# Kernel tuning notes

Hardware: AMD Instinct MI355X
Metric: run time of the kernel (lower is better)

The kernel has to match this reference:

```python
import jax, jax.numpy as jnp
import numpy as np

N_NODES = 50000
N_EDGES = 500000
D_FEAT = 128


def setup_inputs() -> dict:
    key = jax.random.key(0)
    k1, k2 = jax.random.split(key)
    x = jax.random.normal(k1, (N_NODES, D_FEAT), dtype=jnp.float32)
    edge_index = jax.random.randint(k2, (2, N_EDGES), 0, N_NODES, dtype=jnp.int64)
    return {"x": x, "edge_index": edge_index}


def reference(x, edge_index):
    # flow='source_to_target': row = edge_index[0] (source j), col = edge_index[1] (target i)
    row, col = edge_index[0], edge_index[1]
    # message(x_j) = x_j ; aggregate = scatter-add at target indices ; update = identity
    messages = jnp.take(x, row, axis=0)            # [E, D] gather
    out = jax.ops.segment_sum(messages, col, num_segments=x.shape[0])  # [N, D]
    return out
```

## Files before the change

### kernel.cpp

```cpp
#include <hip/hip_runtime.h>
#include <hip/hip_bf16.h>


#define D_FEAT 128
#define MAXDEG 32

typedef unsigned short u16;
typedef unsigned int u32;

__device__ __forceinline__ u16 f2bf(float f) {
    union { __hip_bfloat16 h; u16 u; } c;
    c.h = __float2bfloat16(f);
    return c.u;
}
__device__ __forceinline__ float bflo(u32 u) { return __uint_as_float(u << 16); }
__device__ __forceinline__ float bfhi(u32 u) { return __uint_as_float(u & 0xffff0000u); }

__global__ __launch_bounds__(256) void fused_kernel(const float* __restrict__ x,
                                                    u16* __restrict__ xb, int nf4,
                                                    const int* __restrict__ row,
                                                    const int* __restrict__ col,
                                                    int* __restrict__ cnt,
                                                    u16* __restrict__ srclist,
                                                    int* __restrict__ ovf,
                                                    int* __restrict__ ovfcnt,
                                                    int E, int ovfcap,
                                                    int fill_blocks, int aligned) {
    if ((int)blockIdx.x < fill_blocks) {
        const int t = blockIdx.x * 256 + threadIdx.x;
        const int e0 = t * 4;
        if (e0 >= E) return;
        int d[4], s[4], p[4], ne;
        if (aligned && e0 + 4 <= E) {
            const int4 dv = *reinterpret_cast<const int4*>(col + e0);
            const int4 sv = *reinterpret_cast<const int4*>(row + e0);
            d[0] = dv.x; d[1] = dv.y; d[2] = dv.z; d[3] = dv.w;
            s[0] = sv.x; s[1] = sv.y; s[2] = sv.z; s[3] = sv.w;
            ne = 4;
        } else {
            ne = E - e0; if (ne > 4) ne = 4;
            for (int k = 0; k < ne; ++k) { d[k] = col[e0 + k]; s[k] = row[e0 + k]; }
        }
        #pragma unroll
        for (int k = 0; k < 4; ++k)
            if (k < ne) p[k] = atomicAdd(&cnt[d[k]], 1);
        #pragma unroll
        for (int k = 0; k < 4; ++k) {
            if (k < ne) {
                if (p[k] < MAXDEG) {
                    srclist[(size_t)d[k] * MAXDEG + p[k]] = (u16)s[k];
                } else {
                    int o = atomicAdd(ovfcnt, 1);
                    if (o < ovfcap) { ovf[2 * o] = d[k]; ovf[2 * o + 1] = s[k]; }
                }
            }
        }
    } else {
        const int i = ((int)blockIdx.x - fill_blocks) * 256 + threadIdx.x;
        if (i < nf4) {
            const float4 v = reinterpret_cast<const float4*>(x)[i];
            ushort4 o;
            o.x = f2bf(v.x); o.y = f2bf(v.y); o.z = f2bf(v.z); o.w = f2bf(v.w);
            reinterpret_cast<ushort4*>(xb)[i] = o;
        }
    }
}

__global__ __launch_bounds__(256) void gathers_kernel(const u16* __restrict__ xb,
                                                      const int* __restrict__ cnt,
                                                      const u16* __restrict__ srclist,
                                                      const int* __restrict__ ovf,
                                                      const int* __restrict__ ovfcnt,
                                                      float* __restrict__ out,
                                                      int N, int ovfcap) {
    const int bid   = blockIdx.x;
    const int xcd   = bid & 7;
    const int slice = xcd >> 1;
    const int group = ((bid >> 3) << 1) | (bid & 1);
    const int wav   = threadIdx.x >> 6;
    const int wid   = group * 4 + wav;
    if (wid >= N) return;
    const int lane = threadIdx.x & 63;
    const int q  = lane >> 4;
    const int c2 = lane & 15;

    const int rawdeg = cnt[wid];
    const int deg = rawdeg > MAXDEG ? MAXDEG : rawdeg;
    const u16* bucket = srclist + (size_t)wid * MAXDEG;
    const int bval = (int)bucket[lane & 31];

    const size_t colbase = (size_t)slice * 32 + (size_t)c2 * 2;
    float a0 = 0.f, a1 = 0.f;

    int j = 0;
    for (; j + 8 <= deg; j += 8) {
        const int i0 = __shfl(bval, j + q, 64);
        const int i1 = __shfl(bval, j + 4 + q, 64);
        const u32 w0 = *reinterpret_cast<const u32*>(xb + (size_t)i0 * D_FEAT + colbase);
        const u32 w1 = *reinterpret_cast<const u32*>(xb + (size_t)i1 * D_FEAT + colbase);
        a0 += bflo(w0) + bflo(w1);
        a1 += bfhi(w0) + bfhi(w1);
    }
    if (j + 4 <= deg) {
        const int i0 = __shfl(bval, j + q, 64);
        const u32 w0 = *reinterpret_cast<const u32*>(xb + (size_t)i0 * D_FEAT + colbase);
        a0 += bflo(w0); a1 += bfhi(w0);
        j += 4;
    }
    {
        const int r = deg - j;
        const int i0 = __shfl(bval, j + q, 64);
        if (q < r) {
            const u32 w0 = *reinterpret_cast<const u32*>(xb + (size_t)i0 * D_FEAT + colbase);
            a0 += bflo(w0); a1 += bfhi(w0);
        }
    }

    if (rawdeg > MAXDEG) {
        int novf = *ovfcnt;
        if (novf > ovfcap) novf = ovfcap;
        for (int k = 0; k < novf; ++k) {
            if (ovf[2 * k] == wid && q == 0) {
                const int s = ovf[2 * k + 1];
                const u32 w = *reinterpret_cast<const u32*>(xb + (size_t)s * D_FEAT + colbase);
                a0 += bflo(w); a1 += bfhi(w);
            }
        }
    }

    a0 += __shfl_xor(a0, 16, 64);
    a1 += __shfl_xor(a1, 16, 64);
    a0 += __shfl_xor(a0, 32, 64);
    a1 += __shfl_xor(a1, 32, 64);
    if (q == 0) {
        float* o = out + (size_t)wid * D_FEAT + slice * 32 + c2 * 2;
        *reinterpret_cast<float2*>(o) = make_float2(a0, a1);
    }
}

__global__ void mp_scatter_kernel(const float* __restrict__ x,
                                  const int* __restrict__ row,
                                  const int* __restrict__ col,
                                  float* __restrict__ out, int n_edges) {
    const int t = blockIdx.x * blockDim.x + threadIdx.x;
    const int e = t >> 5;
    const int c = t & 31;
    if (e >= n_edges) return;
    const float4 v = *reinterpret_cast<const float4*>(
        x + (size_t)row[e] * D_FEAT + (size_t)c * 4);
    float* o = out + (size_t)col[e] * D_FEAT + (size_t)c * 4;
    atomicAdd(o + 0, v.x);
    atomicAdd(o + 1, v.y);
    atomicAdd(o + 2, v.z);
    atomicAdd(o + 3, v.w);
}

extern "C" void kernel_launch(void* const* d_in, const int* in_sizes, int n_in,
                              void* d_out, int out_size, void* d_ws, size_t ws_size,
                              hipStream_t stream) {
    const float* x   = (const float*)d_in[0];
    const int*   ei  = (const int*)d_in[1];
    float*       out = (float*)d_out;

    const int E = in_sizes[1] / 2;
    const int N = out_size / D_FEAT;
    const int* row = ei;
    const int* col = ei + E;

    const size_t cnt_bytes = ((size_t)N + 1) * 4;
    const size_t xb_off    = (cnt_bytes + 255) & ~(size_t)255;
    const size_t xb_bytes  = (size_t)N * D_FEAT * 2;
    const size_t src_off   = (xb_off + xb_bytes + 255) & ~(size_t)255;
    const size_t src_bytes = (size_t)N * MAXDEG * 2;
    const size_t ovf_off   = (src_off + src_bytes + 255) & ~(size_t)255;
    const size_t needed    = ovf_off + 2ull * (size_t)E * 4;

    if (ws_size < needed || N > 65535) {
        (void)hipMemsetAsync(d_out, 0, (size_t)out_size * sizeof(float), stream);
        const int total = E * 32;
        mp_scatter_kernel<<<(total + 255) / 256, 256, 0, stream>>>(x, row, col, out, E);
        return;
    }

    char* wsb     = (char*)d_ws;
    int*  cnt     = (int*)wsb;
    int*  ovfcnt  = cnt + N;
    u16*  xb      = (u16*)(wsb + xb_off);
    u16*  srclist = (u16*)(wsb + src_off);
    int*  ovf     = (int*)(wsb + ovf_off);

    (void)hipMemsetAsync(cnt, 0, cnt_bytes, stream);

    const int fill_threads = (E + 3) / 4;
    const int fill_blocks  = (fill_threads + 255) / 256;
    const int nf4          = N * D_FEAT / 4;
    const int conv_blocks  = (nf4 + 255) / 256;
    const int aligned      = ((E & 3) == 0) ? 1 : 0;
    fused_kernel<<<fill_blocks + conv_blocks, 256, 0, stream>>>(
        x, xb, nf4, row, col, cnt, srclist, ovf, ovfcnt, E, E, fill_blocks, aligned);

    const int blocks_per_slice = (N + 3) / 4;
    const int half             = (blocks_per_slice + 1) / 2;
    const int grid             = 8 * half;
    gathers_kernel<<<grid, 256, 0, stream>>>(xb, cnt, srclist, ovf, ovfcnt, out, N, E);
}
```

Before: 151.4 us.

## Widen gather loads to 16-byte per lane and add nontemporal hints

The gather kernel now assigns each lane 8 bf16 columns loaded as one 16-byte vector, with 16 neighbor slots per wavefront iteration instead of 4 slots of 4-byte loads. This cuts the number of memory instructions and loop iterations per node. The cost is a longer cross-lane reduction (8 accumulators over 4 xor-shuffle steps) and more registers. Nontemporal loads and stores are also added for the streamed edge indices, the input conversion and the output writes.

```diff
diff --git a/kernel.cpp b/kernel.cpp
--- a/kernel.cpp
+++ b/kernel.cpp
@@ -7,6 +7,8 @@
 
 typedef unsigned short u16;
 typedef unsigned int u32;
+typedef float  f32x4 __attribute__((ext_vector_type(4)));
+typedef int    i32x4 __attribute__((ext_vector_type(4)));
 
 __device__ __forceinline__ u16 f2bf(float f) {
     union { __hip_bfloat16 h; u16 u; } c;
@@ -32,8 +34,10 @@
         if (e0 >= E) return;
         int d[4], s[4], p[4], ne;
         if (aligned && e0 + 4 <= E) {
-            const int4 dv = *reinterpret_cast<const int4*>(col + e0);
-            const int4 sv = *reinterpret_cast<const int4*>(row + e0);
+            const i32x4 dv = __builtin_nontemporal_load(
+                reinterpret_cast<const i32x4*>(col + e0));
+            const i32x4 sv = __builtin_nontemporal_load(
+                reinterpret_cast<const i32x4*>(row + e0));
             d[0] = dv.x; d[1] = dv.y; d[2] = dv.z; d[3] = dv.w;
             s[0] = sv.x; s[1] = sv.y; s[2] = sv.z; s[3] = sv.w;
             ne = 4;
@@ -58,7 +62,8 @@
     } else {
         const int i = ((int)blockIdx.x - fill_blocks) * 256 + threadIdx.x;
         if (i < nf4) {
-            const float4 v = reinterpret_cast<const float4*>(x)[i];
+            const f32x4 v = __builtin_nontemporal_load(
+                reinterpret_cast<const f32x4*>(x) + i);
             ushort4 o;
             o.x = f2bf(v.x); o.y = f2bf(v.y); o.z = f2bf(v.z); o.w = f2bf(v.w);
             reinterpret_cast<ushort4*>(xb)[i] = o;
@@ -81,38 +86,26 @@
     const int wid   = group * 4 + wav;
     if (wid >= N) return;
     const int lane = threadIdx.x & 63;
-    const int q  = lane >> 4;
-    const int c2 = lane & 15;
+    const int slot = lane >> 2;
+    const int c    = lane & 3;
 
     const int rawdeg = cnt[wid];
     const int deg = rawdeg > MAXDEG ? MAXDEG : rawdeg;
     const u16* bucket = srclist + (size_t)wid * MAXDEG;
     const int bval = (int)bucket[lane & 31];
 
-    const size_t colbase = (size_t)slice * 32 + (size_t)c2 * 2;
-    float a0 = 0.f, a1 = 0.f;
-
-    int j = 0;
-    for (; j + 8 <= deg; j += 8) {
-        const int i0 = __shfl(bval, j + q, 64);
-        const int i1 = __shfl(bval, j + 4 + q, 64);
-        const u32 w0 = *reinterpret_cast<const u32*>(xb + (size_t)i0 * D_FEAT + colbase);
-        const u32 w1 = *reinterpret_cast<const u32*>(xb + (size_t)i1 * D_FEAT + colbase);
-        a0 += bflo(w0) + bflo(w1);
-        a1 += bfhi(w0) + bfhi(w1);
-    }
-    if (j + 4 <= deg) {
-        const int i0 = __shfl(bval, j + q, 64);
-        const u32 w0 = *reinterpret_cast<const u32*>(xb + (size_t)i0 * D_FEAT + colbase);
-        a0 += bflo(w0); a1 += bfhi(w0);
-        j += 4;
-    }
-    {
-        const int r = deg - j;
-        const int i0 = __shfl(bval, j + q, 64);
-        if (q < r) {
-            const u32 w0 = *reinterpret_cast<const u32*>(xb + (size_t)i0 * D_FEAT + colbase);
-            a0 += bflo(w0); a1 += bfhi(w0);
+    const size_t colbase = (size_t)slice * 32 + (size_t)c * 8;
+    float acc[8] = {0.f, 0.f, 0.f, 0.f, 0.f, 0.f, 0.f, 0.f};
+
+    for (int j = 0; j < deg; j += 16) {
+        const int src = __shfl(bval, j + slot, 64);
+        if (j + slot < deg) {
+            const uint4 w = *reinterpret_cast<const uint4*>(
+                xb + (size_t)src * D_FEAT + colbase);
+            acc[0] += bflo(w.x); acc[1] += bfhi(w.x);
+            acc[2] += bflo(w.y); acc[3] += bfhi(w.y);
+            acc[4] += bflo(w.z); acc[5] += bfhi(w.z);
+            acc[6] += bflo(w.w); acc[7] += bfhi(w.w);
         }
     }
 
@@ -120,21 +113,31 @@
         int novf = *ovfcnt;
         if (novf > ovfcap) novf = ovfcap;
         for (int k = 0; k < novf; ++k) {
-            if (ovf[2 * k] == wid && q == 0) {
+            if (ovf[2 * k] == wid && slot == 0) {
                 const int s = ovf[2 * k + 1];
-                const u32 w = *reinterpret_cast<const u32*>(xb + (size_t)s * D_FEAT + colbase);
-                a0 += bflo(w); a1 += bfhi(w);
+                const uint4 w = *reinterpret_cast<const uint4*>(
+                    xb + (size_t)s * D_FEAT + colbase);
+                acc[0] += bflo(w.x); acc[1] += bfhi(w.x);
+                acc[2] += bflo(w.y); acc[3] += bfhi(w.y);
+                acc[4] += bflo(w.z); acc[5] += bfhi(w.z);
+                acc[6] += bflo(w.w); acc[7] += bfhi(w.w);
             }
         }
     }
 
-    a0 += __shfl_xor(a0, 16, 64);
-    a1 += __shfl_xor(a1, 16, 64);
-    a0 += __shfl_xor(a0, 32, 64);
-    a1 += __shfl_xor(a1, 32, 64);
-    if (q == 0) {
-        float* o = out + (size_t)wid * D_FEAT + slice * 32 + c2 * 2;
-        *reinterpret_cast<float2*>(o) = make_float2(a0, a1);
+    #pragma unroll
+    for (int k = 0; k < 8; ++k) {
+        acc[k] += __shfl_xor(acc[k], 4, 64);
+        acc[k] += __shfl_xor(acc[k], 8, 64);
+        acc[k] += __shfl_xor(acc[k], 16, 64);
+        acc[k] += __shfl_xor(acc[k], 32, 64);
+    }
+    if (slot == 0) {
+        float* o = out + (size_t)wid * D_FEAT + slice * 32 + c * 8;
+        f32x4 v0 = {acc[0], acc[1], acc[2], acc[3]};
+        f32x4 v1 = {acc[4], acc[5], acc[6], acc[7]};
+        __builtin_nontemporal_store(v0, reinterpret_cast<f32x4*>(o));
+        __builtin_nontemporal_store(v1, reinterpret_cast<f32x4*>(o + 4));
     }
 }
 
```

Measured after the change: 178.1 us. +17.6%, slower.
